# Optimization experiments

Hardware: AMD Instinct MI355X
Metric: run time of the kernel (lower is better)

## Reference

```python
import jax, jax.numpy as jnp
import numpy as np

NUM_LAYERS = 3
H_DIM = 2048
LN_EPS = 1e-5


def _linear(x, W, b):
    # 1x1x1 Conv3d == linear over the channel axis (last axis here)
    return jnp.einsum('...i,oi->...o', x, W) + b


def setup_inputs() -> dict:
    key = jax.random.key(0)
    ks = jax.random.split(key, 16)
    B, N, Cc, Cl, H = 64, 512, 2048, 2048, H_DIM
    s = 0.02
    inp = {
        'clip': jax.random.normal(ks[0], (B, Cc), jnp.float32),
        'lfb': jax.random.normal(ks[1], (B, N, Cl), jnp.float32),
        'Wc': jax.random.normal(ks[2], (H, Cc), jnp.float32) * s,
        'bc': jnp.zeros((H,), jnp.float32),
        'Wl': jax.random.normal(ks[3], (H, Cl), jnp.float32) * s,
        'bl': jnp.zeros((H,), jnp.float32),
        'Wt': jax.random.normal(ks[4], (H, H), jnp.float32) * s,
        'bt': jnp.zeros((H,), jnp.float32),
        'Wp': jax.random.normal(ks[5], (H, H), jnp.float32) * s,
        'bp': jnp.zeros((H,), jnp.float32),
        'Wg': jax.random.normal(ks[6], (H, H), jnp.float32) * s,
        'bg': jnp.zeros((H,), jnp.float32),
        'Wo': jax.random.normal(ks[7], (H, H), jnp.float32) * s,
        'bo': jnp.zeros((H,), jnp.float32),
    }
    return inp


def reference(clip, lfb, Wc, bc, Wl, bl, Wt, bt, Wp, bp, Wg, bg, Wo, bo):
    H = H_DIM
    scale = 1.0 / jnp.sqrt(jnp.asarray(H, clip.dtype))
    # process_clip / process_lfb (dropout = identity in eval)
    A = _linear(clip, Wc, bc)            # [B, H]
    Bfeat = _linear(lfb, Wl, bl)         # [B, N, H]
    # phi/g are layer-independent (shared weights, fixed Bfeat): hoist out of loop
    phi = _linear(Bfeat, Wp, bp)         # [B, N, H]
    g = _linear(Bfeat, Wg, bg)           # [B, N, H]
    out = A
    for _ in range(NUM_LAYERS):
        theta = _linear(A, Wt, bt)                                  # [B, H]
        scores = jnp.einsum('bh,bnh->bn', theta, phi) * scale       # [B, N]
        p = jax.nn.softmax(scores, axis=-1)                         # [B, N]
        t = jnp.einsum('bnh,bn->bh', g, p)                          # [B, H]
        # F.layer_norm over all non-batch dims (just H here), no affine
        mu = jnp.mean(t, axis=-1, keepdims=True)
        var = jnp.mean(jnp.square(t - mu), axis=-1, keepdims=True)
        ln = (t - mu) / jnp.sqrt(var + LN_EPS)
        h = _linear(jax.nn.relu(ln), Wo, bo)                        # [B, H]
        A = h + A
    out = A  # flattened view of [B, H, 1, 1, 1]
    loss = jnp.asarray(0.0, clip.dtype)  # nl_core returns (out, 0); loss is discarded
    return out, loss
```

## Files before the change

### kernel.cpp

```cpp
#include <hip/hip_runtime.h>

#define Bdim 64
#define Ndim 512
#define Hdim 2048
#define KSPLIT 8
#define NCHUNK 8
#define LNEPS 1e-5f
#define WMAT_ELEMS (Hdim * Hdim)

typedef unsigned short u16;
typedef __attribute__((ext_vector_type(8))) short short8;
typedef __attribute__((ext_vector_type(4))) float f32x4;

__device__ __forceinline__ u16 f2bf(float f) {
    unsigned int u = __float_as_uint(f);
    return (u16)((u + 0x7FFFu + ((u >> 16) & 1u)) >> 16);
}
__device__ __forceinline__ float bf2f(u16 s) {
    return __uint_as_float(((unsigned int)s) << 16);
}

__global__ __launch_bounds__(256)
void convert_w(const float* __restrict__ Wc, const float* __restrict__ Wt,
               const float* __restrict__ Wl, const float* __restrict__ Wg,
               const float* __restrict__ Wo, const float* __restrict__ Wp,
               u16* __restrict__ dst)
{
    __shared__ float L[64][65];
    const int t   = threadIdx.x;
    const int mid = blockIdx.x >> 10;
    const int tb  = blockIdx.x & 1023;
    u16* out = dst + (size_t)mid * WMAT_ELEMS;
    if (mid < 5) {
        const float* src = (mid == 0) ? Wc : (mid == 1) ? Wt : (mid == 2) ? Wl
                         : (mid == 3) ? Wg : Wo;
        const size_t base = (size_t)tb * 4096 + (size_t)t * 16;
#pragma unroll
        for (int i = 0; i < 2; ++i) {
            float4 a = *(const float4*)(src + base + i * 8);
            float4 b = *(const float4*)(src + base + i * 8 + 4);
            short8 s;
            s[0] = (short)f2bf(a.x); s[1] = (short)f2bf(a.y);
            s[2] = (short)f2bf(a.z); s[3] = (short)f2bf(a.w);
            s[4] = (short)f2bf(b.x); s[5] = (short)f2bf(b.y);
            s[6] = (short)f2bf(b.z); s[7] = (short)f2bf(b.w);
            *(short8*)(out + base + i * 8) = s;
        }
    } else {
        const float* src = (mid == 5) ? Wp : Wl;
        const int k0 = (tb & 31) * 64;
        const int o0 = (tb >> 5) * 64;
        const int row = t >> 2;
        const int cq  = t & 3;
#pragma unroll
        for (int i = 0; i < 4; ++i) {
            float4 v = *(const float4*)(src + (size_t)(k0 + row) * Hdim + o0 + cq * 16 + i * 4);
            *(float4*)(&L[row][cq * 16 + i * 4]) = v;
        }
        __syncthreads();
        const int orow = t >> 2;
#pragma unroll
        for (int half = 0; half < 2; ++half) {
            short8 s;
#pragma unroll
            for (int i = 0; i < 8; ++i)
                s[i] = (short)f2bf(L[cq * 16 + half * 8 + i][orow]);
            *(short8*)(out + (size_t)(o0 + orow) * Hdim + k0 + cq * 16 + half * 8) = s;
        }
    }
}

__global__ __launch_bounds__(256)
void mfma_gemv(const float* __restrict__ X, const u16* __restrict__ Wb,
               float* __restrict__ part)
{
    __shared__ short Xs[64][72];
    __shared__ short Ws[64][72];
    const int t  = threadIdx.x;
    const int nt = blockIdx.x & 31;
    const int ks = blockIdx.x >> 5;
    const int o0 = nt * 64;
    const int kb = ks * 256;
    const int wv = t >> 6;
    const int ln = t & 63;
    const int xr = t & 63;
    const int xc = (t >> 6) * 16;
    const int wn = t >> 2;
    const int wk = (t & 3) * 16;

    f32x4 acc[4];
#pragma unroll
    for (int i = 0; i < 4; ++i)
#pragma unroll
        for (int j = 0; j < 4; ++j) acc[i][j] = 0.f;

    float4 px[4];
    uint4  pw[2];
    auto gload = [&](int k0) {
#pragma unroll
        for (int i = 0; i < 4; ++i)
            px[i] = *(const float4*)(X + (size_t)xr * Hdim + k0 + xc + i * 4);
        pw[0] = *(const uint4*)(Wb + (size_t)(o0 + wn) * Hdim + k0 + wk);
        pw[1] = *(const uint4*)(Wb + (size_t)(o0 + wn) * Hdim + k0 + wk + 8);
    };
    auto lstore = [&]() {
#pragma unroll
        for (int i = 0; i < 2; ++i) {
            short8 s;
            s[0] = (short)f2bf(px[i*2].x);   s[1] = (short)f2bf(px[i*2].y);
            s[2] = (short)f2bf(px[i*2].z);   s[3] = (short)f2bf(px[i*2].w);
            s[4] = (short)f2bf(px[i*2+1].x); s[5] = (short)f2bf(px[i*2+1].y);
            s[6] = (short)f2bf(px[i*2+1].z); s[7] = (short)f2bf(px[i*2+1].w);
            *(short8*)(&Xs[xr][xc + i * 8]) = s;
        }
        *(uint4*)(&Ws[wn][wk])     = pw[0];
        *(uint4*)(&Ws[wn][wk + 8]) = pw[1];
    };

    gload(kb);
    for (int c = 0; c < 4; ++c) {
        __syncthreads();
        lstore();
        __syncthreads();
        if (c < 3) gload(kb + (c + 1) * 64);
#pragma unroll
        for (int kstep = 0; kstep < 2; ++kstep) {
            const int kf = kstep * 32 + (ln >> 4) * 8;
            short8 af = *(const short8*)(&Xs[16 * wv + (ln & 15)][kf]);
#pragma unroll
            for (int n4 = 0; n4 < 4; ++n4) {
                short8 bf = *(const short8*)(&Ws[n4 * 16 + (ln & 15)][kf]);
                acc[n4] = __builtin_amdgcn_mfma_f32_16x16x32_bf16(af, bf, acc[n4], 0, 0, 0);
            }
        }
    }
#pragma unroll
    for (int n4 = 0; n4 < 4; ++n4) {
#pragma unroll
        for (int r = 0; r < 4; ++r) {
            const int brow = 16 * wv + (ln >> 4) * 4 + r;
            part[(size_t)(ks * 64 + brow) * Hdim + o0 + n4 * 16 + (ln & 15)] = acc[n4][r];
        }
    }
}

template<int HASBIAS, int ACC, int FINAL>
__global__ __launch_bounds__(256)
void combine(const float* __restrict__ part, const float* __restrict__ bias,
             float* __restrict__ Y, float* __restrict__ out, int has_loss)
{
    const int flat4 = blockIdx.x * 256 + threadIdx.x;
    const size_t e  = (size_t)flat4 * 4;
    const int o     = (int)(e & (Hdim - 1));
    float4 v;
    if (HASBIAS) v = *(const float4*)(bias + o);
    else         v = make_float4(0.f, 0.f, 0.f, 0.f);
#pragma unroll
    for (int s = 0; s < KSPLIT; ++s) {
        float4 p = *(const float4*)(part + (size_t)s * (64 * Hdim) + e);
        v.x += p.x; v.y += p.y; v.z += p.z; v.w += p.w;
    }
    if (ACC) {
        float4 a = *(const float4*)(Y + e);
        v.x += a.x; v.y += a.y; v.z += a.z; v.w += a.w;
    }
    *(float4*)(Y + e) = v;
    if (FINAL) {
        *(float4*)(out + e) = v;
        if (has_loss && flat4 == 0) out[Bdim * Hdim] = 0.f;
    }
}

template<int FIRST>
__global__ __launch_bounds__(256, 4)
void flash_chunk(const float* __restrict__ lfb, const u16* __restrict__ lfb16r,
                 u16* __restrict__ lfb16w, const float* __restrict__ thetal,
                 float scale, u16* __restrict__ up,
                 float* __restrict__ wm, float* __restrict__ wz)
{
    __shared__ u16 T[NCHUNK][Hdim];
    __shared__ float th[Hdim];
    __shared__ float sc[NCHUNK];
    __shared__ float wts[NCHUNK];
    const int t  = threadIdx.x;
    const int b  = blockIdx.x >> 6;
    const int ch = blockIdx.x & 63;
    const size_t nbase = (size_t)b * Ndim + ch * NCHUNK;
#pragma unroll
    for (int i = 0; i < 16; ++i) {
        int flat4 = i * 256 + t;
        int row   = flat4 >> 9;
        int c4    = flat4 & 511;
        if (FIRST) {
            float4 v = *(const float4*)(lfb + (nbase + row) * Hdim + c4 * 4);
            ushort4 u4;
            u4.x = f2bf(v.x); u4.y = f2bf(v.y); u4.z = f2bf(v.z); u4.w = f2bf(v.w);
            *(ushort4*)(&T[row][c4 * 4]) = u4;
            *(ushort4*)(lfb16w + (nbase + row) * Hdim + c4 * 4) = u4;
        } else {
            ushort4 u4 = *(const ushort4*)(lfb16r + (nbase + row) * Hdim + c4 * 4);
            *(ushort4*)(&T[row][c4 * 4]) = u4;
        }
    }
#pragma unroll
    for (int i = 0; i < 2; ++i) {
        int c = (i * 256 + t) * 4;
        float4 v = *(const float4*)(thetal + (size_t)b * Hdim + c);
        *(float4*)(&th[c]) = v;
    }
    __syncthreads();
    const int wv = t >> 6, ln = t & 63;
#pragma unroll
    for (int q = 0; q < 2; ++q) {
        int n = wv * 2 + q;
        float a = 0.f;
#pragma unroll
        for (int i = 0; i < 8; ++i) {
            int c = ln * 4 + i * 256;
            ushort4 x = *(const ushort4*)(&T[n][c]);
            float4 y  = *(const float4*)(&th[c]);
            a += bf2f(x.x) * y.x + bf2f(x.y) * y.y + bf2f(x.z) * y.z + bf2f(x.w) * y.w;
        }
#pragma unroll
        for (int off = 32; off; off >>= 1) a += __shfl_xor(a, off, 64);
        if (ln == 0) sc[n] = a * scale;
    }
    __syncthreads();
    float m = sc[0];
#pragma unroll
    for (int n = 1; n < NCHUNK; ++n) m = fmaxf(m, sc[n]);
    if (t < NCHUNK) wts[t] = expf(sc[t] - m);
    __syncthreads();
    if (t == 0) {
        float z = 0.f;
#pragma unroll
        for (int n = 0; n < NCHUNK; ++n) z += wts[n];
        wm[blockIdx.x] = m;
        wz[blockIdx.x] = z;
    }
#pragma unroll
    for (int i = 0; i < 8; ++i) {
        int c = t + i * 256;
        float a = 0.f;
#pragma unroll
        for (int n = 0; n < NCHUNK; ++n) a += wts[n] * bf2f(T[n][c]);
        up[(size_t)blockIdx.x * Hdim + c] = f2bf(a);
    }
}

__global__ __launch_bounds__(256)
void flash_comb(const u16* __restrict__ up, const float* __restrict__ wm,
                const float* __restrict__ wz, float* __restrict__ u)
{
    __shared__ float mm[64], zz[64], ee[64];
    const int t  = threadIdx.x;
    const int b  = blockIdx.x >> 3;
    const int sl = blockIdx.x & 7;
    if (t < 64) { mm[t] = wm[b * 64 + t]; zz[t] = wz[b * 64 + t]; }
    __syncthreads();
    float mg = mm[0];
#pragma unroll
    for (int i = 1; i < 64; ++i) mg = fmaxf(mg, mm[i]);
    if (t < 64) ee[t] = expf(mm[t] - mg);
    __syncthreads();
    float Z = 0.f;
#pragma unroll
    for (int i = 0; i < 64; ++i) Z += zz[i] * ee[i];
    const float inv = 1.f / Z;
    const int col = sl * 256 + t;
    float a = 0.f;
#pragma unroll 8
    for (int ch = 0; ch < 64; ++ch)
        a += ee[ch] * bf2f(up[(size_t)(b * 64 + ch) * Hdim + col]);
    u[(size_t)b * Hdim + col] = a * inv;
}

__global__ __launch_bounds__(256)
void ln_relu_part(const float* __restrict__ part, const float* __restrict__ bias,
                  float* __restrict__ r)
{
    __shared__ float trow[Hdim];
    __shared__ float red[8];
    const int t = threadIdx.x, b = blockIdx.x;
    float sum = 0.f, sq = 0.f;
#pragma unroll
    for (int i = 0; i < 2; ++i) {
        int c = (i * 256 + t) * 4;
        float4 v = *(const float4*)(bias + c);
#pragma unroll
        for (int s = 0; s < KSPLIT; ++s) {
            float4 p = *(const float4*)(part + ((size_t)(s * 64 + b)) * Hdim + c);
            v.x += p.x; v.y += p.y; v.z += p.z; v.w += p.w;
        }
        *(float4*)(&trow[c]) = v;
        sum += v.x + v.y + v.z + v.w;
        sq  += v.x * v.x + v.y * v.y + v.z * v.z + v.w * v.w;
    }
#pragma unroll
    for (int off = 32; off; off >>= 1) {
        sum += __shfl_xor(sum, off, 64);
        sq  += __shfl_xor(sq,  off, 64);
    }
    if ((t & 63) == 0) { red[t >> 6] = sum; red[4 + (t >> 6)] = sq; }
    __syncthreads();
    sum = red[0] + red[1] + red[2] + red[3];
    sq  = red[4] + red[5] + red[6] + red[7];
    const float mu   = sum * (1.f / Hdim);
    const float var  = sq * (1.f / Hdim) - mu * mu;
    const float rstd = rsqrtf(var + LNEPS);
#pragma unroll
    for (int i = 0; i < 2; ++i) {
        int c = (i * 256 + t) * 4;
        float4 v = *(const float4*)(&trow[c]);
        float4 o;
        o.x = fmaxf(0.f, (v.x - mu) * rstd);
        o.y = fmaxf(0.f, (v.y - mu) * rstd);
        o.z = fmaxf(0.f, (v.z - mu) * rstd);
        o.w = fmaxf(0.f, (v.w - mu) * rstd);
        *(float4*)(r + (size_t)b * Hdim + c) = o;
    }
}

extern "C" void kernel_launch(void* const* d_in, const int* in_sizes, int n_in,
                              void* d_out, int out_size, void* d_ws, size_t ws_size,
                              hipStream_t stream) {
    (void)in_sizes; (void)n_in; (void)ws_size;
    const float* clip = (const float*)d_in[0];
    const float* lfb  = (const float*)d_in[1];
    const float* Wc   = (const float*)d_in[2];
    const float* bc   = (const float*)d_in[3];
    const float* Wl   = (const float*)d_in[4];
    const float* bl   = (const float*)d_in[5];
    const float* Wt   = (const float*)d_in[6];
    const float* bt   = (const float*)d_in[7];
    const float* Wp   = (const float*)d_in[8];
    const float* Wg   = (const float*)d_in[10];
    const float* bg   = (const float*)d_in[11];
    const float* Wo   = (const float*)d_in[12];
    const float* bo   = (const float*)d_in[13];
    float* out = (float*)d_out;

    float* wsf    = (float*)d_ws;
    float* A      = wsf;
    float* theta  = wsf + 131072;
    float* thetap = wsf + 262144;
    float* thetal = wsf + 393216;
    float* u      = wsf + 524288;
    float* r      = wsf + 655360;
    float* PA     = wsf + 786432;
    float* wm     = wsf + 1835008;
    float* wz     = wsf + 1839104;
    u16*   up     = (u16*)(wsf + 1843200);
    u16*   lfb16  = (u16*)(wsf + 6037504);
    u16*   Wbf    = (u16*)(wsf + 39591936);

    u16* bWc  = Wbf + (size_t)0 * WMAT_ELEMS;
    u16* bWt  = Wbf + (size_t)1 * WMAT_ELEMS;
    u16* bWl  = Wbf + (size_t)2 * WMAT_ELEMS;
    u16* bWg  = Wbf + (size_t)3 * WMAT_ELEMS;
    u16* bWo  = Wbf + (size_t)4 * WMAT_ELEMS;
    u16* bWpT = Wbf + (size_t)5 * WMAT_ELEMS;
    u16* bWlT = Wbf + (size_t)6 * WMAT_ELEMS;

    const float scale = 0.022097086912079608f;
    dim3 blk(256);
    const int has_loss = (out_size > Bdim * Hdim) ? 1 : 0;

    convert_w<<<7168, blk, 0, stream>>>(Wc, Wt, Wl, Wg, Wo, Wp, Wbf);

    mfma_gemv<<<256, blk, 0, stream>>>(clip, bWc, PA);
    combine<1,0,0><<<128, blk, 0, stream>>>(PA, bc, A, nullptr, 0);

    for (int l = 0; l < 3; ++l) {
        mfma_gemv<<<256, blk, 0, stream>>>(A, bWt, PA);
        combine<1,0,0><<<128, blk, 0, stream>>>(PA, bt, theta, nullptr, 0);
        mfma_gemv<<<256, blk, 0, stream>>>(theta, bWpT, PA);
        combine<0,0,0><<<128, blk, 0, stream>>>(PA, nullptr, thetap, nullptr, 0);
        mfma_gemv<<<256, blk, 0, stream>>>(thetap, bWlT, PA);
        combine<0,0,0><<<128, blk, 0, stream>>>(PA, nullptr, thetal, nullptr, 0);
        if (l == 0)
            flash_chunk<1><<<4096, blk, 0, stream>>>(lfb, nullptr, lfb16, thetal, scale, up, wm, wz);
        else
            flash_chunk<0><<<4096, blk, 0, stream>>>(nullptr, lfb16, nullptr, thetal, scale, up, wm, wz);
        flash_comb<<<512, blk, 0, stream>>>(up, wm, wz, u);
        mfma_gemv<<<256, blk, 0, stream>>>(u, bWl, PA);
        combine<1,0,0><<<128, blk, 0, stream>>>(PA, bl, theta, nullptr, 0);
        mfma_gemv<<<256, blk, 0, stream>>>(theta, bWg, PA);
        ln_relu_part<<<64, blk, 0, stream>>>(PA, bg, r);
        mfma_gemv<<<256, blk, 0, stream>>>(r, bWo, PA);
        if (l < 2)
            combine<1,1,0><<<128, blk, 0, stream>>>(PA, bo, A, nullptr, 0);
        else
            combine<1,1,1><<<128, blk, 0, stream>>>(PA, bo, A, out, has_loss);
    }
}
```

Baseline: 408.6 us.

## Fuse split-K reduction into consumer GEMV loads and pass bf16 activations

Drops most standalone combine kernels. The next GEMV (or flash_chunk) now sums the split-K partials plus bias itself while loading its input tile. Activations that feed the GEMVs directly (A, clip, u, r) are written as bf16, so the GEMV loads them without conversion. This removes roughly four launches per layer and the intermediate float round-trips. In exchange, each consumer tile reads 8x the partial data, repeated across the 32 column-tile blocks, so redundant global traffic rises.

```diff
diff --git a/kernel.cpp b/kernel.cpp
--- a/kernel.cpp
+++ b/kernel.cpp
@@ -24,16 +24,18 @@
 void convert_w(const float* __restrict__ Wc, const float* __restrict__ Wt,
                const float* __restrict__ Wl, const float* __restrict__ Wg,
                const float* __restrict__ Wo, const float* __restrict__ Wp,
-               u16* __restrict__ dst)
+               const float* __restrict__ clip,
+               u16* __restrict__ dst, u16* __restrict__ clip16)
 {
     __shared__ float L[64][65];
     const int t   = threadIdx.x;
-    const int mid = blockIdx.x >> 10;
-    const int tb  = blockIdx.x & 1023;
-    u16* out = dst + (size_t)mid * WMAT_ELEMS;
-    if (mid < 5) {
+    const int bid = blockIdx.x;
+    if (bid < 5120) {
+        const int mid = bid >> 10;
+        const int tb  = bid & 1023;
         const float* src = (mid == 0) ? Wc : (mid == 1) ? Wt : (mid == 2) ? Wl
                          : (mid == 3) ? Wg : Wo;
+        u16* out = dst + (size_t)mid * WMAT_ELEMS;
         const size_t base = (size_t)tb * 4096 + (size_t)t * 16;
 #pragma unroll
         for (int i = 0; i < 2; ++i) {
@@ -46,8 +48,11 @@
             s[6] = (short)f2bf(b.z); s[7] = (short)f2bf(b.w);
             *(short8*)(out + base + i * 8) = s;
         }
-    } else {
+    } else if (bid < 7168) {
+        const int mid = 5 + ((bid - 5120) >> 10);
+        const int tb  = (bid - 5120) & 1023;
         const float* src = (mid == 5) ? Wp : Wl;
+        u16* out = dst + (size_t)mid * WMAT_ELEMS;
         const int k0 = (tb & 31) * 64;
         const int o0 = (tb >> 5) * 64;
         const int row = t >> 2;
@@ -67,11 +72,27 @@
                 s[i] = (short)f2bf(L[cq * 16 + half * 8 + i][orow]);
             *(short8*)(out + (size_t)(o0 + orow) * Hdim + k0 + cq * 16 + half * 8) = s;
         }
-    }
-}
-
+    } else {
+        const int tb = bid - 7168;
+        const size_t base = (size_t)tb * 4096 + (size_t)t * 16;
+#pragma unroll
+        for (int i = 0; i < 2; ++i) {
+            float4 a = *(const float4*)(clip + base + i * 8);
+            float4 b = *(const float4*)(clip + base + i * 8 + 4);
+            short8 s;
+            s[0] = (short)f2bf(a.x); s[1] = (short)f2bf(a.y);
+            s[2] = (short)f2bf(a.z); s[3] = (short)f2bf(a.w);
+            s[4] = (short)f2bf(b.x); s[5] = (short)f2bf(b.y);
+            s[6] = (short)f2bf(b.z); s[7] = (short)f2bf(b.w);
+            *(short8*)(clip16 + base + i * 8) = s;
+        }
+    }
+}
+
+template<int XPART, int XBIAS>
 __global__ __launch_bounds__(256)
-void mfma_gemv(const float* __restrict__ X, const u16* __restrict__ Wb,
+void mfma_gemv(const u16* __restrict__ X16, const float* __restrict__ Xp,
+               const float* __restrict__ xbias, const u16* __restrict__ Wb,
                float* __restrict__ part)
 {
     __shared__ short Xs[64][72];
@@ -84,7 +105,7 @@
     const int wv = t >> 6;
     const int ln = t & 63;
     const int xr = t & 63;
-    const int xc = (t >> 6) * 16;
+    const int xg = t >> 6;
     const int wn = t >> 2;
     const int wk = (t & 3) * 16;
 
@@ -94,24 +115,45 @@
 #pragma unroll
         for (int j = 0; j < 4; ++j) acc[i][j] = 0.f;
 
+    uint4  qx[2];
     float4 px[4];
     uint4  pw[2];
     auto gload = [&](int k0) {
-#pragma unroll
-        for (int i = 0; i < 4; ++i)
-            px[i] = *(const float4*)(X + (size_t)xr * Hdim + k0 + xc + i * 4);
+        if (!XPART) {
+            qx[0] = *(const uint4*)(X16 + (size_t)xr * Hdim + k0 + xg * 16);
+            qx[1] = *(const uint4*)(X16 + (size_t)xr * Hdim + k0 + xg * 16 + 8);
+        } else {
+#pragma unroll
+            for (int i = 0; i < 4; ++i) {
+                if (XBIAS) px[i] = *(const float4*)(xbias + k0 + xg * 16 + i * 4);
+                else       px[i] = make_float4(0.f, 0.f, 0.f, 0.f);
+            }
+#pragma unroll 4
+            for (int s = 0; s < KSPLIT; ++s) {
+#pragma unroll
+                for (int i = 0; i < 4; ++i) {
+                    float4 p = *(const float4*)(Xp + (size_t)(s * 64 + xr) * Hdim + k0 + xg * 16 + i * 4);
+                    px[i].x += p.x; px[i].y += p.y; px[i].z += p.z; px[i].w += p.w;
+                }
+            }
+        }
         pw[0] = *(const uint4*)(Wb + (size_t)(o0 + wn) * Hdim + k0 + wk);
         pw[1] = *(const uint4*)(Wb + (size_t)(o0 + wn) * Hdim + k0 + wk + 8);
     };
     auto lstore = [&]() {
-#pragma unroll
-        for (int i = 0; i < 2; ++i) {
-            short8 s;
-            s[0] = (short)f2bf(px[i*2].x);   s[1] = (short)f2bf(px[i*2].y);
-            s[2] = (short)f2bf(px[i*2].z);   s[3] = (short)f2bf(px[i*2].w);
-            s[4] = (short)f2bf(px[i*2+1].x); s[5] = (short)f2bf(px[i*2+1].y);
-            s[6] = (short)f2bf(px[i*2+1].z); s[7] = (short)f2bf(px[i*2+1].w);
-            *(short8*)(&Xs[xr][xc + i * 8]) = s;
+        if (!XPART) {
+            *(uint4*)(&Xs[xr][xg * 16])     = qx[0];
+            *(uint4*)(&Xs[xr][xg * 16 + 8]) = qx[1];
+        } else {
+#pragma unroll
+            for (int i = 0; i < 2; ++i) {
+                short8 s;
+                s[0] = (short)f2bf(px[i*2].x);   s[1] = (short)f2bf(px[i*2].y);
+                s[2] = (short)f2bf(px[i*2].z);   s[3] = (short)f2bf(px[i*2].w);
+                s[4] = (short)f2bf(px[i*2+1].x); s[5] = (short)f2bf(px[i*2+1].y);
+                s[6] = (short)f2bf(px[i*2+1].z); s[7] = (short)f2bf(px[i*2+1].w);
+                *(short8*)(&Xs[xr][xg * 16 + i * 8]) = s;
+            }
         }
         *(uint4*)(&Ws[wn][wk])     = pw[0];
         *(uint4*)(&Ws[wn][wk + 8]) = pw[1];
@@ -144,17 +186,16 @@
     }
 }
 
-template<int HASBIAS, int ACC, int FINAL>
+template<int ACC, int FINAL>
 __global__ __launch_bounds__(256)
 void combine(const float* __restrict__ part, const float* __restrict__ bias,
-             float* __restrict__ Y, float* __restrict__ out, int has_loss)
+             float* __restrict__ Y, u16* __restrict__ Y16,
+             float* __restrict__ out, int has_loss)
 {
     const int flat4 = blockIdx.x * 256 + threadIdx.x;
     const size_t e  = (size_t)flat4 * 4;
     const int o     = (int)(e & (Hdim - 1));
-    float4 v;
-    if (HASBIAS) v = *(const float4*)(bias + o);
-    else         v = make_float4(0.f, 0.f, 0.f, 0.f);
+    float4 v = *(const float4*)(bias + o);
 #pragma unroll
     for (int s = 0; s < KSPLIT; ++s) {
         float4 p = *(const float4*)(part + (size_t)s * (64 * Hdim) + e);
@@ -165,6 +206,9 @@
         v.x += a.x; v.y += a.y; v.z += a.z; v.w += a.w;
     }
     *(float4*)(Y + e) = v;
+    ushort4 m;
+    m.x = f2bf(v.x); m.y = f2bf(v.y); m.z = f2bf(v.z); m.w = f2bf(v.w);
+    *(ushort4*)(Y16 + e) = m;
     if (FINAL) {
         *(float4*)(out + e) = v;
         if (has_loss && flat4 == 0) out[Bdim * Hdim] = 0.f;
@@ -174,7 +218,7 @@
 template<int FIRST>
 __global__ __launch_bounds__(256, 4)
 void flash_chunk(const float* __restrict__ lfb, const u16* __restrict__ lfb16r,
-                 u16* __restrict__ lfb16w, const float* __restrict__ thetal,
+                 u16* __restrict__ lfb16w, const float* __restrict__ thpart,
                  float scale, u16* __restrict__ up,
                  float* __restrict__ wm, float* __restrict__ wz)
 {
@@ -205,7 +249,12 @@
 #pragma unroll
     for (int i = 0; i < 2; ++i) {
         int c = (i * 256 + t) * 4;
-        float4 v = *(const float4*)(thetal + (size_t)b * Hdim + c);
+        float4 v = make_float4(0.f, 0.f, 0.f, 0.f);
+#pragma unroll
+        for (int s = 0; s < KSPLIT; ++s) {
+            float4 p = *(const float4*)(thpart + (size_t)(s * 64 + b) * Hdim + c);
+            v.x += p.x; v.y += p.y; v.z += p.z; v.w += p.w;
+        }
         *(float4*)(&th[c]) = v;
     }
     __syncthreads();
@@ -250,7 +299,7 @@
 
 __global__ __launch_bounds__(256)
 void flash_comb(const u16* __restrict__ up, const float* __restrict__ wm,
-                const float* __restrict__ wz, float* __restrict__ u)
+                const float* __restrict__ wz, u16* __restrict__ u16out)
 {
     __shared__ float mm[64], zz[64], ee[64];
     const int t  = threadIdx.x;
@@ -272,12 +321,12 @@
 #pragma unroll 8
     for (int ch = 0; ch < 64; ++ch)
         a += ee[ch] * bf2f(up[(size_t)(b * 64 + ch) * Hdim + col]);
-    u[(size_t)b * Hdim + col] = a * inv;
+    u16out[(size_t)b * Hdim + col] = f2bf(a * inv);
 }
 
 __global__ __launch_bounds__(256)
 void ln_relu_part(const float* __restrict__ part, const float* __restrict__ bias,
-                  float* __restrict__ r)
+                  u16* __restrict__ r16)
 {
     __shared__ float trow[Hdim];
     __shared__ float red[8];
@@ -312,12 +361,12 @@
     for (int i = 0; i < 2; ++i) {
         int c = (i * 256 + t) * 4;
         float4 v = *(const float4*)(&trow[c]);
-        float4 o;
-        o.x = fmaxf(0.f, (v.x - mu) * rstd);
-        o.y = fmaxf(0.f, (v.y - mu) * rstd);
-        o.z = fmaxf(0.f, (v.z - mu) * rstd);
-        o.w = fmaxf(0.f, (v.w - mu) * rstd);
-        *(float4*)(r + (size_t)b * Hdim + c) = o;
+        ushort4 o;
+        o.x = f2bf(fmaxf(0.f, (v.x - mu) * rstd));
+        o.y = f2bf(fmaxf(0.f, (v.y - mu) * rstd));
+        o.z = f2bf(fmaxf(0.f, (v.z - mu) * rstd));
+        o.w = f2bf(fmaxf(0.f, (v.w - mu) * rstd));
+        *(ushort4*)(r16 + (size_t)b * Hdim + c) = o;
     }
 }
 
@@ -342,17 +391,17 @@
 
     float* wsf    = (float*)d_ws;
     float* A      = wsf;
-    float* theta  = wsf + 131072;
-    float* thetap = wsf + 262144;
-    float* thetal = wsf + 393216;
-    float* u      = wsf + 524288;
-    float* r      = wsf + 655360;
-    float* PA     = wsf + 786432;
-    float* wm     = wsf + 1835008;
-    float* wz     = wsf + 1839104;
-    u16*   up     = (u16*)(wsf + 1843200);
-    u16*   lfb16  = (u16*)(wsf + 6037504);
-    u16*   Wbf    = (u16*)(wsf + 39591936);
+    u16*   A16    = (u16*)(wsf + 131072);
+    u16*   ubuf   = (u16*)(wsf + 196608);
+    u16*   r16    = (u16*)(wsf + 262144);
+    u16*   clip16 = (u16*)(wsf + 327680);
+    float* wm     = wsf + 393216;
+    float* wz     = wsf + 397312;
+    float* PA     = wsf + 401408;
+    float* PB     = wsf + 1449984;
+    u16*   up     = (u16*)(wsf + 2498560);
+    u16*   lfb16  = (u16*)(wsf + 6692864);
+    u16*   Wbf    = (u16*)(wsf + 40247296);
 
     u16* bWc  = Wbf + (size_t)0 * WMAT_ELEMS;
     u16* bWt  = Wbf + (size_t)1 * WMAT_ELEMS;
@@ -366,31 +415,27 @@
     dim3 blk(256);
     const int has_loss = (out_size > Bdim * Hdim) ? 1 : 0;
 
-    convert_w<<<7168, blk, 0, stream>>>(Wc, Wt, Wl, Wg, Wo, Wp, Wbf);
-
-    mfma_gemv<<<256, blk, 0, stream>>>(clip, bWc, PA);
-    combine<1,0,0><<<128, blk, 0, stream>>>(PA, bc, A, nullptr, 0);
+    convert_w<<<7200, blk, 0, stream>>>(Wc, Wt, Wl, Wg, Wo, Wp, clip, Wbf, clip16);
+
+    mfma_gemv<0,0><<<256, blk, 0, stream>>>(clip16, nullptr, nullptr, bWc, PA);
+    combine<0,0><<<128, blk, 0, stream>>>(PA, bc, A, A16, nullptr, 0);
 
     for (int l = 0; l < 3; ++l) {
-        mfma_gemv<<<256, blk, 0, stream>>>(A, bWt, PA);
-        combine<1,0,0><<<128, blk, 0, stream>>>(PA, bt, theta, nullptr, 0);
-        mfma_gemv<<<256, blk, 0, stream>>>(theta, bWpT, PA);
-        combine<0,0,0><<<128, blk, 0, stream>>>(PA, nullptr, thetap, nullptr, 0);
-        mfma_gemv<<<256, blk, 0, stream>>>(thetap, bWlT, PA);
-        combine<0,0,0><<<128, blk, 0, stream>>>(PA, nullptr, thetal, nullptr, 0);
+        mfma_gemv<0,0><<<256, blk, 0, stream>>>(A16, nullptr, nullptr, bWt, PA);
+        mfma_gemv<1,1><<<256, blk, 0, stream>>>(nullptr, PA, bt, bWpT, PB);
+        mfma_gemv<1,0><<<256, blk, 0, stream>>>(nullptr, PB, nullptr, bWlT, PA);
         if (l == 0)
-            flash_chunk<1><<<4096, blk, 0, stream>>>(lfb, nullptr, lfb16, thetal, scale, up, wm, wz);
+            flash_chunk<1><<<4096, blk, 0, stream>>>(lfb, nullptr, lfb16, PA, scale, up, wm, wz);
         else
-            flash_chunk<0><<<4096, blk, 0, stream>>>(nullptr, lfb16, nullptr, thetal, scale, up, wm, wz);
-        flash_comb<<<512, blk, 0, stream>>>(up, wm, wz, u);
-        mfma_gemv<<<256, blk, 0, stream>>>(u, bWl, PA);
-        combine<1,0,0><<<128, blk, 0, stream>>>(PA, bl, theta, nullptr, 0);
-        mfma_gemv<<<256, blk, 0, stream>>>(theta, bWg, PA);
-        ln_relu_part<<<64, blk, 0, stream>>>(PA, bg, r);
-        mfma_gemv<<<256, blk, 0, stream>>>(r, bWo, PA);
+            flash_chunk<0><<<4096, blk, 0, stream>>>(nullptr, lfb16, nullptr, PA, scale, up, wm, wz);
+        flash_comb<<<512, blk, 0, stream>>>(up, wm, wz, ubuf);
+        mfma_gemv<0,0><<<256, blk, 0, stream>>>(ubuf, nullptr, nullptr, bWl, PB);
+        mfma_gemv<1,1><<<256, blk, 0, stream>>>(nullptr, PB, bl, bWg, PA);
+        ln_relu_part<<<64, blk, 0, stream>>>(PA, bg, r16);
+        mfma_gemv<0,0><<<256, blk, 0, stream>>>(r16, nullptr, nullptr, bWo, PB);
         if (l < 2)
-            combine<1,1,0><<<128, blk, 0, stream>>>(PA, bo, A, nullptr, 0);
+            combine<1,0><<<128, blk, 0, stream>>>(PB, bo, A, A16, nullptr, 0);
         else
-            combine<1,1,1><<<128, blk, 0, stream>>>(PA, bo, A, out, has_loss);
-    }
-}
+            combine<1,1><<<128, blk, 0, stream>>>(PB, bo, A, A16, out, has_loss);
+    }
+}
```

New measurement: 520.9 us. 1.28x slower.

## Drop split-K GEMV partials, fuse bias/residual epilogue and emit bf16 activations

Applied to the files above, without the earlier changes.

The GEMV kernel now does the full K reduction per block with 32-wide output tiles and double-buffered 128-wide K chunks. Bias, residual add and the final output write move into its epilogue, which removes the separate combine kernels and the partial-sum buffer traffic. Producers now write bf16 copies of activations (clip is converted in the weight-conversion kernel), so the GEMV loads bf16 directly with no in-kernel conversion. The cost is that only 64 blocks run per GEMV, each with a long serial K loop, which may underfill the GPU.

```diff
diff --git a/kernel.cpp b/kernel.cpp
--- a/kernel.cpp
+++ b/kernel.cpp
@@ -3,10 +3,11 @@
 #define Bdim 64
 #define Ndim 512
 #define Hdim 2048
-#define KSPLIT 8
 #define NCHUNK 8
 #define LNEPS 1e-5f
 #define WMAT_ELEMS (Hdim * Hdim)
+#define OTILE 32
+#define KC 128
 
 typedef unsigned short u16;
 typedef __attribute__((ext_vector_type(8))) short short8;
@@ -24,16 +25,18 @@
 void convert_w(const float* __restrict__ Wc, const float* __restrict__ Wt,
                const float* __restrict__ Wl, const float* __restrict__ Wg,
                const float* __restrict__ Wo, const float* __restrict__ Wp,
-               u16* __restrict__ dst)
+               const float* __restrict__ clip,
+               u16* __restrict__ dst, u16* __restrict__ clip16)
 {
     __shared__ float L[64][65];
     const int t   = threadIdx.x;
-    const int mid = blockIdx.x >> 10;
-    const int tb  = blockIdx.x & 1023;
-    u16* out = dst + (size_t)mid * WMAT_ELEMS;
-    if (mid < 5) {
+    const int bid = blockIdx.x;
+    if (bid < 5120) {
+        const int mid = bid >> 10;
+        const int tb  = bid & 1023;
         const float* src = (mid == 0) ? Wc : (mid == 1) ? Wt : (mid == 2) ? Wl
                          : (mid == 3) ? Wg : Wo;
+        u16* out = dst + (size_t)mid * WMAT_ELEMS;
         const size_t base = (size_t)tb * 4096 + (size_t)t * 16;
 #pragma unroll
         for (int i = 0; i < 2; ++i) {
@@ -46,8 +49,11 @@
             s[6] = (short)f2bf(b.z); s[7] = (short)f2bf(b.w);
             *(short8*)(out + base + i * 8) = s;
         }
-    } else {
+    } else if (bid < 7168) {
+        const int mid = 5 + ((bid - 5120) >> 10);
+        const int tb  = (bid - 5120) & 1023;
         const float* src = (mid == 5) ? Wp : Wl;
+        u16* out = dst + (size_t)mid * WMAT_ELEMS;
         const int k0 = (tb & 31) * 64;
         const int o0 = (tb >> 5) * 64;
         const int row = t >> 2;
@@ -67,108 +73,98 @@
                 s[i] = (short)f2bf(L[cq * 16 + half * 8 + i][orow]);
             *(short8*)(out + (size_t)(o0 + orow) * Hdim + k0 + cq * 16 + half * 8) = s;
         }
-    }
-}
-
+    } else {
+        const int tb = bid - 7168;
+        const size_t base = (size_t)tb * 4096 + (size_t)t * 16;
+#pragma unroll
+        for (int i = 0; i < 2; ++i) {
+            float4 a = *(const float4*)(clip + base + i * 8);
+            float4 b = *(const float4*)(clip + base + i * 8 + 4);
+            short8 s;
+            s[0] = (short)f2bf(a.x); s[1] = (short)f2bf(a.y);
+            s[2] = (short)f2bf(a.z); s[3] = (short)f2bf(a.w);
+            s[4] = (short)f2bf(b.x); s[5] = (short)f2bf(b.y);
+            s[6] = (short)f2bf(b.z); s[7] = (short)f2bf(b.w);
+            *(short8*)(clip16 + base + i * 8) = s;
+        }
+    }
+}
+
+template<int HASBIAS, int ACC, int FINAL>
 __global__ __launch_bounds__(256)
-void mfma_gemv(const float* __restrict__ X, const u16* __restrict__ Wb,
-               float* __restrict__ part)
-{
-    __shared__ short Xs[64][72];
-    __shared__ short Ws[64][72];
+void mfma_gemv(const u16* __restrict__ X16, const u16* __restrict__ Wb,
+               const float* __restrict__ bias,
+               float* __restrict__ Y, u16* __restrict__ Y16,
+               float* __restrict__ out, int has_loss)
+{
+    __shared__ short Xs[2][64][136];
+    __shared__ short Ws[2][OTILE][136];
     const int t  = threadIdx.x;
-    const int nt = blockIdx.x & 31;
-    const int ks = blockIdx.x >> 5;
-    const int o0 = nt * 64;
-    const int kb = ks * 256;
+    const int o0 = blockIdx.x * OTILE;
     const int wv = t >> 6;
     const int ln = t & 63;
     const int xr = t & 63;
-    const int xc = (t >> 6) * 16;
-    const int wn = t >> 2;
-    const int wk = (t & 3) * 16;
-
-    f32x4 acc[4];
-#pragma unroll
-    for (int i = 0; i < 4; ++i)
+    const int xg = t >> 6;
+    const int wn = t >> 3;
+    const int wk = (t & 7) * 16;
+
+    f32x4 acc[2];
+#pragma unroll
+    for (int i = 0; i < 2; ++i)
 #pragma unroll
         for (int j = 0; j < 4; ++j) acc[i][j] = 0.f;
 
-    float4 px[4];
-    uint4  pw[2];
+    uint4 qx[4], qw[2];
     auto gload = [&](int k0) {
 #pragma unroll
         for (int i = 0; i < 4; ++i)
-            px[i] = *(const float4*)(X + (size_t)xr * Hdim + k0 + xc + i * 4);
-        pw[0] = *(const uint4*)(Wb + (size_t)(o0 + wn) * Hdim + k0 + wk);
-        pw[1] = *(const uint4*)(Wb + (size_t)(o0 + wn) * Hdim + k0 + wk + 8);
+            qx[i] = *(const uint4*)(X16 + (size_t)xr * Hdim + k0 + xg * 32 + i * 8);
+        qw[0] = *(const uint4*)(Wb + (size_t)(o0 + wn) * Hdim + k0 + wk);
+        qw[1] = *(const uint4*)(Wb + (size_t)(o0 + wn) * Hdim + k0 + wk + 8);
     };
-    auto lstore = [&]() {
-#pragma unroll
-        for (int i = 0; i < 2; ++i) {
-            short8 s;
-            s[0] = (short)f2bf(px[i*2].x);   s[1] = (short)f2bf(px[i*2].y);
-            s[2] = (short)f2bf(px[i*2].z);   s[3] = (short)f2bf(px[i*2].w);
-            s[4] = (short)f2bf(px[i*2+1].x); s[5] = (short)f2bf(px[i*2+1].y);
-            s[6] = (short)f2bf(px[i*2+1].z); s[7] = (short)f2bf(px[i*2+1].w);
-            *(short8*)(&Xs[xr][xc + i * 8]) = s;
-        }
-        *(uint4*)(&Ws[wn][wk])     = pw[0];
-        *(uint4*)(&Ws[wn][wk + 8]) = pw[1];
+    auto lstore = [&](int buf) {
+#pragma unroll
+        for (int i = 0; i < 4; ++i)
+            *(uint4*)(&Xs[buf][xr][xg * 32 + i * 8]) = qx[i];
+        *(uint4*)(&Ws[buf][wn][wk])     = qw[0];
+        *(uint4*)(&Ws[buf][wn][wk + 8]) = qw[1];
     };
 
-    gload(kb);
-    for (int c = 0; c < 4; ++c) {
-        __syncthreads();
-        lstore();
-        __syncthreads();
-        if (c < 3) gload(kb + (c + 1) * 64);
-#pragma unroll
-        for (int kstep = 0; kstep < 2; ++kstep) {
+    gload(0);
+    lstore(0);
+    __syncthreads();
+    for (int c = 0; c < 16; ++c) {
+        const int cur = c & 1;
+        if (c < 15) gload((c + 1) * KC);
+#pragma unroll
+        for (int kstep = 0; kstep < 4; ++kstep) {
             const int kf = kstep * 32 + (ln >> 4) * 8;
-            short8 af = *(const short8*)(&Xs[16 * wv + (ln & 15)][kf]);
-#pragma unroll
-            for (int n4 = 0; n4 < 4; ++n4) {
-                short8 bf = *(const short8*)(&Ws[n4 * 16 + (ln & 15)][kf]);
+            short8 af = *(const short8*)(&Xs[cur][16 * wv + (ln & 15)][kf]);
+#pragma unroll
+            for (int n4 = 0; n4 < 2; ++n4) {
+                short8 bf = *(const short8*)(&Ws[cur][n4 * 16 + (ln & 15)][kf]);
                 acc[n4] = __builtin_amdgcn_mfma_f32_16x16x32_bf16(af, bf, acc[n4], 0, 0, 0);
             }
         }
-    }
-#pragma unroll
-    for (int n4 = 0; n4 < 4; ++n4) {
+        if (c < 15) lstore(cur ^ 1);
+        __syncthreads();
+    }
+#pragma unroll
+    for (int n4 = 0; n4 < 2; ++n4) {
+        const int col = o0 + n4 * 16 + (ln & 15);
+        float bv = 0.f;
+        if (HASBIAS) bv = bias[col];
 #pragma unroll
         for (int r = 0; r < 4; ++r) {
-            const int brow = 16 * wv + (ln >> 4) * 4 + r;
-            part[(size_t)(ks * 64 + brow) * Hdim + o0 + n4 * 16 + (ln & 15)] = acc[n4][r];
-        }
-    }
-}
-
-template<int HASBIAS, int ACC, int FINAL>
-__global__ __launch_bounds__(256)
-void combine(const float* __restrict__ part, const float* __restrict__ bias,
-             float* __restrict__ Y, float* __restrict__ out, int has_loss)
-{
-    const int flat4 = blockIdx.x * 256 + threadIdx.x;
-    const size_t e  = (size_t)flat4 * 4;
-    const int o     = (int)(e & (Hdim - 1));
-    float4 v;
-    if (HASBIAS) v = *(const float4*)(bias + o);
-    else         v = make_float4(0.f, 0.f, 0.f, 0.f);
-#pragma unroll
-    for (int s = 0; s < KSPLIT; ++s) {
-        float4 p = *(const float4*)(part + (size_t)s * (64 * Hdim) + e);
-        v.x += p.x; v.y += p.y; v.z += p.z; v.w += p.w;
-    }
-    if (ACC) {
-        float4 a = *(const float4*)(Y + e);
-        v.x += a.x; v.y += a.y; v.z += a.z; v.w += a.w;
-    }
-    *(float4*)(Y + e) = v;
-    if (FINAL) {
-        *(float4*)(out + e) = v;
-        if (has_loss && flat4 == 0) out[Bdim * Hdim] = 0.f;
-    }
+            const int row = 16 * wv + (ln >> 4) * 4 + r;
+            float v = acc[n4][r] + bv;
+            if (ACC) v += Y[(size_t)row * Hdim + col];
+            Y[(size_t)row * Hdim + col] = v;
+            Y16[(size_t)row * Hdim + col] = f2bf(v);
+            if (FINAL) out[(size_t)row * Hdim + col] = v;
+        }
+    }
+    if (FINAL && has_loss && t == 0 && blockIdx.x == 0) out[Bdim * Hdim] = 0.f;
 }
 
 template<int FIRST>
@@ -250,7 +246,7 @@
 
 __global__ __launch_bounds__(256)
 void flash_comb(const u16* __restrict__ up, const float* __restrict__ wm,
-                const float* __restrict__ wz, float* __restrict__ u)
+                const float* __restrict__ wz, u16* __restrict__ u16out)
 {
     __shared__ float mm[64], zz[64], ee[64];
     const int t  = threadIdx.x;
@@ -272,30 +268,19 @@
 #pragma unroll 8
     for (int ch = 0; ch < 64; ++ch)
         a += ee[ch] * bf2f(up[(size_t)(b * 64 + ch) * Hdim + col]);
-    u[(size_t)b * Hdim + col] = a * inv;
+    u16out[(size_t)b * Hdim + col] = f2bf(a * inv);
 }
 
 __global__ __launch_bounds__(256)
-void ln_relu_part(const float* __restrict__ part, const float* __restrict__ bias,
-                  float* __restrict__ r)
-{
-    __shared__ float trow[Hdim];
+void ln_relu(const float* __restrict__ tin, u16* __restrict__ r16)
+{
     __shared__ float red[8];
     const int t = threadIdx.x, b = blockIdx.x;
-    float sum = 0.f, sq = 0.f;
-#pragma unroll
-    for (int i = 0; i < 2; ++i) {
-        int c = (i * 256 + t) * 4;
-        float4 v = *(const float4*)(bias + c);
-#pragma unroll
-        for (int s = 0; s < KSPLIT; ++s) {
-            float4 p = *(const float4*)(part + ((size_t)(s * 64 + b)) * Hdim + c);
-            v.x += p.x; v.y += p.y; v.z += p.z; v.w += p.w;
-        }
-        *(float4*)(&trow[c]) = v;
-        sum += v.x + v.y + v.z + v.w;
-        sq  += v.x * v.x + v.y * v.y + v.z * v.z + v.w * v.w;
-    }
+    float4 v0 = *(const float4*)(tin + (size_t)b * Hdim + t * 4);
+    float4 v1 = *(const float4*)(tin + (size_t)b * Hdim + (256 + t) * 4);
+    float sum = v0.x + v0.y + v0.z + v0.w + v1.x + v1.y + v1.z + v1.w;
+    float sq  = v0.x*v0.x + v0.y*v0.y + v0.z*v0.z + v0.w*v0.w
+              + v1.x*v1.x + v1.y*v1.y + v1.z*v1.z + v1.w*v1.w;
 #pragma unroll
     for (int off = 32; off; off >>= 1) {
         sum += __shfl_xor(sum, off, 64);
@@ -308,17 +293,17 @@
     const float mu   = sum * (1.f / Hdim);
     const float var  = sq * (1.f / Hdim) - mu * mu;
     const float rstd = rsqrtf(var + LNEPS);
-#pragma unroll
-    for (int i = 0; i < 2; ++i) {
-        int c = (i * 256 + t) * 4;
-        float4 v = *(const float4*)(&trow[c]);
-        float4 o;
-        o.x = fmaxf(0.f, (v.x - mu) * rstd);
-        o.y = fmaxf(0.f, (v.y - mu) * rstd);
-        o.z = fmaxf(0.f, (v.z - mu) * rstd);
-        o.w = fmaxf(0.f, (v.w - mu) * rstd);
-        *(float4*)(r + (size_t)b * Hdim + c) = o;
-    }
+    ushort4 o0, o1;
+    o0.x = f2bf(fmaxf(0.f, (v0.x - mu) * rstd));
+    o0.y = f2bf(fmaxf(0.f, (v0.y - mu) * rstd));
+    o0.z = f2bf(fmaxf(0.f, (v0.z - mu) * rstd));
+    o0.w = f2bf(fmaxf(0.f, (v0.w - mu) * rstd));
+    o1.x = f2bf(fmaxf(0.f, (v1.x - mu) * rstd));
+    o1.y = f2bf(fmaxf(0.f, (v1.y - mu) * rstd));
+    o1.z = f2bf(fmaxf(0.f, (v1.z - mu) * rstd));
+    o1.w = f2bf(fmaxf(0.f, (v1.w - mu) * rstd));
+    *(ushort4*)(r16 + (size_t)b * Hdim + t * 4)         = o0;
+    *(ushort4*)(r16 + (size_t)b * Hdim + (256 + t) * 4) = o1;
 }
 
 extern "C" void kernel_launch(void* const* d_in, const int* in_sizes, int n_in,
@@ -342,17 +327,22 @@
 
     float* wsf    = (float*)d_ws;
     float* A      = wsf;
-    float* theta  = wsf + 131072;
-    float* thetap = wsf + 262144;
-    float* thetal = wsf + 393216;
-    float* u      = wsf + 524288;
-    float* r      = wsf + 655360;
-    float* PA     = wsf + 786432;
-    float* wm     = wsf + 1835008;
-    float* wz     = wsf + 1839104;
-    u16*   up     = (u16*)(wsf + 1843200);
-    u16*   lfb16  = (u16*)(wsf + 6037504);
-    u16*   Wbf    = (u16*)(wsf + 39591936);
+    float* thetal = wsf + 131072;
+    float* tY     = wsf + 262144;
+    float* scrY   = wsf + 393216;
+    u16*   A16    = (u16*)(wsf + 524288);
+    u16*   th16   = (u16*)(wsf + 589824);
+    u16*   tp16   = (u16*)(wsf + 655360);
+    u16*   s16    = (u16*)(wsf + 720896);
+    u16*   ubuf   = (u16*)(wsf + 786432);
+    u16*   r16    = (u16*)(wsf + 851968);
+    u16*   clip16 = (u16*)(wsf + 917504);
+    u16*   junk16 = (u16*)(wsf + 983040);
+    float* wm     = wsf + 1048576;
+    float* wz     = wsf + 1052672;
+    u16*   up     = (u16*)(wsf + 1056768);
+    u16*   lfb16  = (u16*)(wsf + 5251072);
+    u16*   Wbf    = (u16*)(wsf + 38805504);
 
     u16* bWc  = Wbf + (size_t)0 * WMAT_ELEMS;
     u16* bWt  = Wbf + (size_t)1 * WMAT_ELEMS;
@@ -366,31 +356,25 @@
     dim3 blk(256);
     const int has_loss = (out_size > Bdim * Hdim) ? 1 : 0;
 
-    convert_w<<<7168, blk, 0, stream>>>(Wc, Wt, Wl, Wg, Wo, Wp, Wbf);
-
-    mfma_gemv<<<256, blk, 0, stream>>>(clip, bWc, PA);
-    combine<1,0,0><<<128, blk, 0, stream>>>(PA, bc, A, nullptr, 0);
+    convert_w<<<7200, blk, 0, stream>>>(Wc, Wt, Wl, Wg, Wo, Wp, clip, Wbf, clip16);
+
+    mfma_gemv<1,0,0><<<64, blk, 0, stream>>>(clip16, bWc, bc, A, A16, nullptr, 0);
 
     for (int l = 0; l < 3; ++l) {
-        mfma_gemv<<<256, blk, 0, stream>>>(A, bWt, PA);
-        combine<1,0,0><<<128, blk, 0, stream>>>(PA, bt, theta, nullptr, 0);
-        mfma_gemv<<<256, blk, 0, stream>>>(theta, bWpT, PA);
-        combine<0,0,0><<<128, blk, 0, stream>>>(PA, nullptr, thetap, nullptr, 0);
-        mfma_gemv<<<256, blk, 0, stream>>>(thetap, bWlT, PA);
-        combine<0,0,0><<<128, blk, 0, stream>>>(PA, nullptr, thetal, nullptr, 0);
+        mfma_gemv<1,0,0><<<64, blk, 0, stream>>>(A16, bWt, bt, scrY, th16, nullptr, 0);
+        mfma_gemv<0,0,0><<<64, blk, 0, stream>>>(th16, bWpT, nullptr, scrY, tp16, nullptr, 0);
+        mfma_gemv<0,0,0><<<64, blk, 0, stream>>>(tp16, bWlT, nullptr, thetal, junk16, nullptr, 0);
         if (l == 0)
             flash_chunk<1><<<4096, blk, 0, stream>>>(lfb, nullptr, lfb16, thetal, scale, up, wm, wz);
         else
             flash_chunk<0><<<4096, blk, 0, stream>>>(nullptr, lfb16, nullptr, thetal, scale, up, wm, wz);
-        flash_comb<<<512, blk, 0, stream>>>(up, wm, wz, u);
-        mfma_gemv<<<256, blk, 0, stream>>>(u, bWl, PA);
-        combine<1,0,0><<<128, blk, 0, stream>>>(PA, bl, theta, nullptr, 0);
-        mfma_gemv<<<256, blk, 0, stream>>>(theta, bWg, PA);
-        ln_relu_part<<<64, blk, 0, stream>>>(PA, bg, r);
-        mfma_gemv<<<256, blk, 0, stream>>>(r, bWo, PA);
+        flash_comb<<<512, blk, 0, stream>>>(up, wm, wz, ubuf);
+        mfma_gemv<1,0,0><<<64, blk, 0, stream>>>(ubuf, bWl, bl, scrY, s16, nullptr, 0);
+        mfma_gemv<1,0,0><<<64, blk, 0, stream>>>(s16, bWg, bg, tY, junk16, nullptr, 0);
+        ln_relu<<<64, blk, 0, stream>>>(tY, r16);
         if (l < 2)
-            combine<1,1,0><<<128, blk, 0, stream>>>(PA, bo, A, nullptr, 0);
+            mfma_gemv<1,1,0><<<64, blk, 0, stream>>>(r16, bWo, bo, A, A16, nullptr, 0);
         else
-            combine<1,1,1><<<128, blk, 0, stream>>>(PA, bo, A, out, has_loss);
-    }
-}
+            mfma_gemv<1,1,1><<<64, blk, 0, stream>>>(r16, bWo, bo, A, A16, out, has_loss);
+    }
+}
```

Result: slower. 801.8 us (+96.2%).
